# Performance work log

Measured on AMD Instinct MI355X. Metric: run time of the kernel, lower is better.

The kernel has to match this reference:

```python
import jax, jax.numpy as jnp
import numpy as np

D_MODEL = 1024
D_STATE = 16
D_CONV = 4
EXPAND = 2
D_INNER = EXPAND * D_MODEL
BATCH = 2
SEQ = 4096


def setup_inputs() -> dict:
    key = jax.random.key(0)
    ks = jax.random.split(key, 8)
    def w(k, shape, fan_in):
        return jax.random.normal(k, shape, jnp.float32) * (fan_in ** -0.5)
    x = jax.random.normal(ks[0], (BATCH, SEQ, D_MODEL), jnp.float32)
    in_proj_w = w(ks[1], (2 * D_INNER, D_MODEL), D_MODEL)
    conv_w = w(ks[2], (D_INNER, 1, D_CONV), D_CONV)          # depthwise conv kernel (OIH, groups=D_INNER)
    conv_b = jnp.zeros((D_INNER,), jnp.float32)
    x_proj_w = w(ks[3], (1 + 2 * D_STATE, D_INNER), D_INNER)
    dt_proj_w = w(ks[4], (D_INNER, 1), D_STATE)               # Linear(1 -> d_inner), see notes
    dt_proj_b = jnp.zeros((D_INNER,), jnp.float32)
    A_log = jnp.log(jnp.tile(jnp.arange(1, D_STATE + 1, dtype=jnp.float32)[None, :], (D_INNER, 1)))
    D = jnp.ones((D_INNER,), jnp.float32)
    out_proj_w = w(ks[5], (D_MODEL, D_INNER), D_INNER)
    return dict(x=x, in_proj_w=in_proj_w, conv_w=conv_w, conv_b=conv_b,
                x_proj_w=x_proj_w, dt_proj_w=dt_proj_w, dt_proj_b=dt_proj_b,
                A_log=A_log, D=D, out_proj_w=out_proj_w)


def _selective_scan(xs, delta, Bm, Cm, A, D):
    # xs, delta: [B, L, d_inner]; Bm, Cm: [B, L, d_state]; A: [d_inner, d_state]
    def step(h, inp):
        x_t, d_t, b_t, c_t = inp                      # [B,di],[B,di],[B,n],[B,n]
        dA = jnp.exp(d_t[..., None] * A)              # [B, di, n]
        h = dA * h + (d_t * x_t)[..., None] * b_t[:, None, :]
        y = jnp.einsum('bdn,bn->bd', h, c_t) + D * x_t
        return h, y
    h0 = jnp.zeros((xs.shape[0], xs.shape[2], A.shape[1]), xs.dtype)
    seq = (jnp.swapaxes(xs, 0, 1), jnp.swapaxes(delta, 0, 1),
           jnp.swapaxes(Bm, 0, 1), jnp.swapaxes(Cm, 0, 1))
    _, ys = jax.lax.scan(step, h0, seq)               # ys: [L, B, di]
    return jnp.swapaxes(ys, 0, 1)


def _mamba(x, in_proj_w, conv_w, conv_b, x_proj_w, dt_proj_w, dt_proj_b, A_log, D, out_proj_w):
    xz = x @ in_proj_w.T                               # [B, L, 2*di]
    xc, z = jnp.split(xz, 2, axis=-1)
    # causal depthwise conv (pad left d_conv-1, truncate to seq_len)
    u = jnp.swapaxes(xc, 1, 2)                         # [B, di, L]
    u = jax.lax.conv_general_dilated(
        u, conv_w, window_strides=(1,), padding=[(D_CONV - 1, 0)],
        feature_group_count=D_INNER, dimension_numbers=('NCH', 'OIH', 'NCH'))
    u = u + conv_b[None, :, None]
    xs = jax.nn.silu(jnp.swapaxes(u, 1, 2))            # [B, L, di]
    dbc = xs @ x_proj_w.T                              # [B, L, 1+2n]
    delta_raw = dbc[..., :1]
    Bm = dbc[..., 1:1 + D_STATE]
    Cm = dbc[..., 1 + D_STATE:]
    delta = jax.nn.softplus(delta_raw @ dt_proj_w.T + dt_proj_b)   # [B, L, di]
    A = -jnp.exp(A_log)
    y = _selective_scan(xs, delta, Bm, Cm, A, D)
    return (y * jax.nn.silu(z)) @ out_proj_w.T


def reference(x, in_proj_w, conv_w, conv_b, x_proj_w, dt_proj_w, dt_proj_b, A_log, D, out_proj_w):
    return _mamba(x, in_proj_w, conv_w, conv_b, x_proj_w, dt_proj_w, dt_proj_b, A_log, D, out_proj_w)
```

## Files before the change

### kernel.cpp

```cpp
#include <hip/hip_runtime.h>
#include <hip/hip_bf16.h>
#include <stdint.h>

typedef __bf16 bf16x8 __attribute__((ext_vector_type(8)));
typedef float  f32x4  __attribute__((ext_vector_type(4)));
typedef unsigned short u16x8 __attribute__((ext_vector_type(8)));

#define TC 64
#define NC 64
#define TH 32

__device__ __forceinline__ unsigned short f2bf(float f) {
  unsigned u = __builtin_bit_cast(unsigned, f);
  unsigned r = (u + 0x7fffu + ((u >> 16) & 1u)) >> 16;
  return (unsigned short)r;
}
__device__ __forceinline__ float bf2f(unsigned short s) {
  unsigned u = ((unsigned)s) << 16;
  return __builtin_bit_cast(float, u);
}

__device__ __forceinline__ void gload_lds16(const void* g, void* l) {
  __builtin_amdgcn_global_load_lds(
      (const __attribute__((address_space(1))) unsigned int*)(g),
      (__attribute__((address_space(3))) unsigned int*)(l),
      16, 0, 0);
}

__device__ __forceinline__ void rpowers(float r, float* rp) {
  float r2 = r * r, r4 = r2 * r2, r8 = r4 * r4;
  rp[0] = r;        rp[1] = r2;       rp[2] = r2 * r;   rp[3] = r4;
  rp[4] = r4 * r;   rp[5] = r4 * r2;  rp[6] = rp[5] * r; rp[7] = r8;
  rp[8] = r8 * r;   rp[9] = r8 * r2;  rp[10] = rp[9] * r; rp[11] = r8 * r4;
  rp[12] = rp[11] * r; rp[13] = rp[11] * r2; rp[14] = rp[13] * r; rp[15] = r8 * r8;
}

__global__ __launch_bounds__(256) void cast_bf16_k(const float4* __restrict__ in,
                                                   ushort4* __restrict__ out, int n4) {
  int i = blockIdx.x * 256 + threadIdx.x;
  int stride = gridDim.x * 256;
  for (; i < n4; i += stride) {
    float4 v = in[i];
    ushort4 o;
    o.x = f2bf(v.x); o.y = f2bf(v.y); o.z = f2bf(v.z); o.w = f2bf(v.w);
    out[i] = o;
  }
}

__global__ __launch_bounds__(256) void pad_xw_k(const float* __restrict__ xw,
                                                unsigned short* __restrict__ xwp) {
  int i = blockIdx.x * 256 + threadIdx.x;
  if (i >= 128 * 2048) return;
  int row = i >> 11, col = i & 2047;
  xwp[i] = (row < 33) ? f2bf(xw[row * 2048 + col]) : (unsigned short)0;
}

template <bool BF16OUT, bool SWZ>
__global__ __launch_bounds__(256) void gemm2p(
    const unsigned short* __restrict__ A, const unsigned short* __restrict__ B,
    void* __restrict__ Cv, int M, int N, int K)
{
  __shared__ __align__(16) unsigned short AsB[3 * 128 * 32];
  __shared__ __align__(16) unsigned short BsB[3 * 128 * 32];
  const int tid = threadIdx.x;

  const int grid_m = M >> 7, grid_n = N >> 7;
  const int nwg = grid_m * grid_n;
  int wid = blockIdx.x;
  if (SWZ) { int q = nwg >> 3; wid = (wid & 7) * q + (wid >> 3); }
  const int GM = 16;
  const int nig = GM * grid_n;
  const int gidg = wid / nig;
  const int rem = wid - gidg * nig;
  const int fm = gidg * GM;
  const int gsz = min(grid_m - fm, GM);
  const int pm = fm + rem % gsz;
  const int pn = rem / gsz;
  const int m0 = pm << 7, n0 = pn << 7;

  const int kseg = K / gridDim.z;
  const int kbeg = blockIdx.z * kseg;
  const int NT = kseg >> 5;

  const int w = tid >> 6, l = tid & 63;
  const int wr = w >> 1, wc = w & 1;
  const int lr = l & 15, kk = (l >> 4) * 8;

  f32x4 acc[4][4];
#pragma unroll
  for (int mi = 0; mi < 4; ++mi)
#pragma unroll
    for (int ni = 0; ni < 4; ++ni)
      acc[mi][ni] = (f32x4){0.f, 0.f, 0.f, 0.f};

#pragma unroll
  for (int tt = 0; tt < 2; ++tt) {
    unsigned short* as = AsB + tt * 4096;
    unsigned short* bs = BsB + tt * 4096;
    int k0 = kbeg + tt * 32;
#pragma unroll
    for (int i = 0; i < 2; ++i) {
      int q = tid + 256 * i;
      int row = q >> 2, sub = (q & 3) ^ ((q >> 3) & 3);
      gload_lds16(A + (size_t)(m0 + row) * K + k0 + sub * 8, as + q * 8);
      gload_lds16(B + (size_t)(n0 + row) * K + k0 + sub * 8, bs + q * 8);
    }
  }
  asm volatile("s_waitcnt vmcnt(4)\n\ts_barrier" ::: "memory");

  for (int t = 0; t < NT; ++t) {
    if (t + 2 < NT) {
      unsigned short* as = AsB + ((t + 2) % 3) * 4096;
      unsigned short* bs = BsB + ((t + 2) % 3) * 4096;
      int k0 = kbeg + (t + 2) * 32;
#pragma unroll
      for (int i = 0; i < 2; ++i) {
        int q = tid + 256 * i;
        int row = q >> 2, sub = (q & 3) ^ ((q >> 3) & 3);
        gload_lds16(A + (size_t)(m0 + row) * K + k0 + sub * 8, as + q * 8);
        gload_lds16(B + (size_t)(n0 + row) * K + k0 + sub * 8, bs + q * 8);
      }
    }
    const unsigned short* as = AsB + (t % 3) * 4096;
    const unsigned short* bs = BsB + (t % 3) * 4096;
    bf16x8 af[4], bfr[4];
#pragma unroll
    for (int mi = 0; mi < 4; ++mi) {
      int row = wr * 64 + mi * 16 + lr;
      int col = kk ^ (((row >> 1) & 3) << 3);
      af[mi] = *(const bf16x8*)&as[row * 32 + col];
    }
#pragma unroll
    for (int ni = 0; ni < 4; ++ni) {
      int row = wc * 64 + ni * 16 + lr;
      int col = kk ^ (((row >> 1) & 3) << 3);
      bfr[ni] = *(const bf16x8*)&bs[row * 32 + col];
    }
    __builtin_amdgcn_s_setprio(1);
#pragma unroll
    for (int mi = 0; mi < 4; ++mi)
#pragma unroll
      for (int ni = 0; ni < 4; ++ni)
        acc[mi][ni] = __builtin_amdgcn_mfma_f32_16x16x32_bf16(af[mi], bfr[ni], acc[mi][ni], 0, 0, 0);
    __builtin_amdgcn_s_setprio(0);
    if (t + 1 < NT) {
      if (t + 2 < NT) asm volatile("s_waitcnt vmcnt(4)\n\ts_barrier" ::: "memory");
      else            asm volatile("s_waitcnt vmcnt(0)\n\ts_barrier" ::: "memory");
    }
  }

#pragma unroll
  for (int mi = 0; mi < 4; ++mi)
#pragma unroll
    for (int ni = 0; ni < 4; ++ni) {
      int gr = m0 + wr * 64 + mi * 16 + (l >> 4) * 4;
      int gc = n0 + wc * 64 + ni * 16 + (l & 15);
#pragma unroll
      for (int j = 0; j < 4; ++j) {
        if (BF16OUT)
          ((unsigned short*)Cv)[(size_t)(gr + j) * N + gc] = f2bf(acc[mi][ni][j]);
        else
          ((float*)Cv + (size_t)blockIdx.z * M * N)[(size_t)(gr + j) * N + gc] = acc[mi][ni][j];
      }
    }
}

__global__ __launch_bounds__(256) void redux4_k(const float4* __restrict__ part,
                                                float4* __restrict__ out) {
  int i = blockIdx.x * 256 + threadIdx.x;
  const int STR = 262144;
  float4 a = part[i], b = part[i + STR], c = part[i + 2 * STR], d = part[i + 3 * STR];
  out[i] = make_float4(a.x + b.x + c.x + d.x, a.y + b.y + c.y + d.y,
                       a.z + b.z + c.z + d.z, a.w + b.w + c.w + d.w);
}

#define CONV_L 16
__global__ __launch_bounds__(256) void conv_silu_k(
    const unsigned short* __restrict__ xzb, const float* __restrict__ cw,
    const float* __restrict__ cb, unsigned short* __restrict__ xsb)
{
  const int b = blockIdx.y;
  const int l0 = blockIdx.x * CONV_L;
  const int d = threadIdx.x * 8;
  float w[4][8], bias[8];
#pragma unroll
  for (int i = 0; i < 8; ++i) {
    bias[i] = cb[d + i];
#pragma unroll
    for (int j = 0; j < 4; ++j) w[j][i] = cw[(d + i) * 4 + j];
  }
  const size_t rb = (size_t)b * 4096;
  float win[3][8];
#pragma unroll
  for (int j = 0; j < 3; ++j) {
    int l = l0 - 3 + j;
    if (l >= 0) {
      u16x8 v = *(const u16x8*)(xzb + (rb + l) * 4096 + d);
#pragma unroll
      for (int i = 0; i < 8; ++i) win[j][i] = bf2f(v[i]);
    } else {
#pragma unroll
      for (int i = 0; i < 8; ++i) win[j][i] = 0.f;
    }
  }
  for (int l = l0; l < l0 + CONV_L; ++l) {
    u16x8 v = *(const u16x8*)(xzb + (rb + l) * 4096 + d);
    float cur[8]; u16x8 ob;
#pragma unroll
    for (int i = 0; i < 8; ++i) {
      cur[i] = bf2f(v[i]);
      float u = bias[i] + w[0][i] * win[0][i] + w[1][i] * win[1][i]
                        + w[2][i] * win[2][i] + w[3][i] * cur[i];
      float s = u / (1.f + __expf(-u));
      ob[i] = f2bf(s);
    }
    *(u16x8*)(xsb + (rb + l) * 2048 + d) = ob;
#pragma unroll
    for (int i = 0; i < 8; ++i) { win[0][i] = win[1][i]; win[1][i] = win[2][i]; win[2][i] = cur[i]; }
  }
}

__global__ __launch_bounds__(256) void scan_p1(
    const unsigned short* __restrict__ xsb16, const float* __restrict__ dbc,
    const float* __restrict__ dtw, const float* __restrict__ dtb,
    const float* __restrict__ alog,
    float* __restrict__ Sg, float* __restrict__ cdg)
{
  const int chunk = blockIdx.x;
  const int d0 = blockIdx.y * 256;
  const int b = blockIdx.z;
  const int tid = threadIdx.x;
  const size_t rowbase = (size_t)b * 4096 + chunk * TC;

  __shared__ __align__(16) unsigned short xsS[TH][256];
  __shared__ __align__(16) float bS[TC][16];
  __shared__ float drS[TC];

  if (tid < TC) drS[tid] = dbc[(rowbase + tid) * 128];
  for (int i = tid; i < TC * 16; i += 256) {
    int t = i >> 4, q = i & 15;
    bS[t][q] = dbc[(rowbase + t) * 128 + 1 + q];
  }

  const int d = d0 + tid;
  const float wdt = dtw[d], bdt = dtb[d];
  float adn[16];
  bool ok = true;
#pragma unroll
  for (int k = 0; k < 4; ++k) {
    float4 a4 = *(const float4*)(alog + (size_t)d * 16 + k * 4);
    adn[4 * k + 0] = -__expf(a4.x); adn[4 * k + 1] = -__expf(a4.y);
    adn[4 * k + 2] = -__expf(a4.z); adn[4 * k + 3] = -__expf(a4.w);
  }
#pragma unroll
  for (int n = 0; n < 16; ++n)
    ok = ok && (fabsf(adn[n] + (float)(n + 1)) <= 1e-3f * (float)(n + 1));

  float h[16];
#pragma unroll
  for (int n = 0; n < 16; ++n) h[n] = 0.f;
  float cd = 0.f;

  for (int half = 0; half < 2; ++half) {
    if (half) __syncthreads();
    for (int i = tid; i < TH * 32; i += 256) {
      int tt = i >> 5, q = i & 31;
      *(u16x8*)&xsS[tt][q * 8] =
          *(const u16x8*)(xsb16 + (rowbase + half * TH + tt) * 2048 + d0 + q * 8);
    }
    __syncthreads();

    if (ok) {
      for (int tt = 0; tt < TH; ++tt) {
        int t = half * TH + tt;
        float pre = fmaf(drS[t], wdt, bdt);
        float e = __expf(pre);
        float dlt = (pre > 20.f) ? pre : __logf(1.f + e);
        float xv = bf2f(xsS[tt][tid]);
        float dx = dlt * xv;
        cd += dlt;
        float r = __expf(-dlt);
        float rp[16];
        rpowers(r, rp);
        f32x4 Bv[4];
#pragma unroll
        for (int k = 0; k < 4; ++k) Bv[k] = ((const f32x4*)&bS[t][0])[k];
#pragma unroll
        for (int n = 0; n < 16; ++n)
          h[n] = fmaf(rp[n], h[n], dx * Bv[n >> 2][n & 3]);
      }
    } else {
      for (int tt = 0; tt < TH; ++tt) {
        int t = half * TH + tt;
        float pre = fmaf(drS[t], wdt, bdt);
        float e = __expf(pre);
        float dlt = (pre > 20.f) ? pre : __logf(1.f + e);
        float xv = bf2f(xsS[tt][tid]);
        float dx = dlt * xv;
        cd += dlt;
        f32x4 Bv[4];
#pragma unroll
        for (int k = 0; k < 4; ++k) Bv[k] = ((const f32x4*)&bS[t][0])[k];
#pragma unroll
        for (int n = 0; n < 16; ++n) {
          float dA = __expf(adn[n] * dlt);
          h[n] = fmaf(dA, h[n], dx * Bv[n >> 2][n & 3]);
        }
      }
    }
  }
  cdg[(size_t)(b * NC + chunk) * 2048 + d] = cd;
  float* Sp = Sg + ((size_t)(b * NC + chunk) * 32768 + (size_t)d * 16);
#pragma unroll
  for (int k = 0; k < 4; ++k)
    ((float4*)Sp)[k] = make_float4(h[4 * k], h[4 * k + 1], h[4 * k + 2], h[4 * k + 3]);
}

__global__ __launch_bounds__(256) void scan_p2(
    const float* __restrict__ Sg, const float* __restrict__ cdg,
    const float* __restrict__ alog, float* __restrict__ Hg)
{
  int g = blockIdx.x * 256 + threadIdx.x;
  int b = g >> 15, dn = g & 32767;
  int d = dn >> 4;
  float adn = -__expf(alog[dn]);
  float h = 0.f;
  for (int c = 0; c < NC; ++c) {
    size_t o = (size_t)(b * NC + c) * 32768 + dn;
    float P = __expf(adn * cdg[(size_t)(b * NC + c) * 2048 + d]);
    Hg[o] = h;
    h = fmaf(P, h, Sg[o]);
  }
}

__global__ __launch_bounds__(256) void scan_p3(
    const unsigned short* __restrict__ xsb16, const float* __restrict__ dbc,
    const float* __restrict__ dtw, const float* __restrict__ dtb,
    const float* __restrict__ alog, const float* __restrict__ Dp,
    const unsigned short* __restrict__ xzb, const float* __restrict__ Hg,
    unsigned short* __restrict__ gb)
{
  const int chunk = blockIdx.x;
  const int d0 = blockIdx.y * 256;
  const int b = blockIdx.z;
  const int tid = threadIdx.x;
  const size_t rowbase = (size_t)b * 4096 + chunk * TC;

  __shared__ __align__(16) unsigned short xsS[TH][256];
  __shared__ __align__(16) float bcS[TC][32];

  for (int i = tid; i < TC * 32; i += 256) {
    int t = i >> 5, q = i & 31;
    bcS[t][q] = dbc[(rowbase + t) * 128 + 1 + q];
  }

  const int d = d0 + tid;
  const float wdt = dtw[d], bdt = dtb[d], Dd = Dp[d];
  const float* __restrict__ drp = dbc + rowbase * 128;
  float adn[16];
  bool ok = true;
#pragma unroll
  for (int k = 0; k < 4; ++k) {
    float4 a4 = *(const float4*)(alog + (size_t)d * 16 + k * 4);
    adn[4 * k + 0] = -__expf(a4.x); adn[4 * k + 1] = -__expf(a4.y);
    adn[4 * k + 2] = -__expf(a4.z); adn[4 * k + 3] = -__expf(a4.w);
  }
#pragma unroll
  for (int n = 0; n < 16; ++n)
    ok = ok && (fabsf(adn[n] + (float)(n + 1)) <= 1e-3f * (float)(n + 1));

  float h[16];
  {
    const float* Hp = Hg + ((size_t)(b * NC + chunk) * 32768 + (size_t)d * 16);
#pragma unroll
    for (int k = 0; k < 4; ++k) {
      float4 h4 = ((const float4*)Hp)[k];
      h[4 * k + 0] = h4.x; h[4 * k + 1] = h4.y; h[4 * k + 2] = h4.z; h[4 * k + 3] = h4.w;
    }
  }

  for (int half = 0; half < 2; ++half) {
    if (half) __syncthreads();
    for (int i = tid; i < TH * 32; i += 256) {
      int tt = i >> 5, q = i & 31;
      *(u16x8*)&xsS[tt][q * 8] =
          *(const u16x8*)(xsb16 + (rowbase + half * TH + tt) * 2048 + d0 + q * 8);
    }
    __syncthreads();

    if (ok) {
      for (int tt = 0; tt < TH; ++tt) {
        int t = half * TH + tt;
        float pre = fmaf(drp[(size_t)t * 128], wdt, bdt);
        float e = __expf(pre);
        float dlt = (pre > 20.f) ? pre : __logf(1.f + e);
        float xv = bf2f(xsS[tt][tid]);
        float dx = dlt * xv;
        float r = __expf(-dlt);
        float rp[16];
        rpowers(r, rp);
        f32x4 Bv[4], Cv[4];
#pragma unroll
        for (int k = 0; k < 4; ++k) {
          Bv[k] = ((const f32x4*)&bcS[t][0])[k];
          Cv[k] = ((const f32x4*)&bcS[t][16])[k];
        }
        float yp[4];
        yp[0] = Dd * xv; yp[1] = 0.f; yp[2] = 0.f; yp[3] = 0.f;
#pragma unroll
        for (int n = 0; n < 16; ++n) {
          h[n] = fmaf(rp[n], h[n], dx * Bv[n >> 2][n & 3]);
          yp[n & 3] = fmaf(h[n], Cv[n >> 2][n & 3], yp[n & 3]);
        }
        float y = (yp[0] + yp[1]) + (yp[2] + yp[3]);
        xsS[tt][tid] = f2bf(y);
      }
    } else {
      for (int tt = 0; tt < TH; ++tt) {
        int t = half * TH + tt;
        float pre = fmaf(drp[(size_t)t * 128], wdt, bdt);
        float e = __expf(pre);
        float dlt = (pre > 20.f) ? pre : __logf(1.f + e);
        float xv = bf2f(xsS[tt][tid]);
        float dx = dlt * xv;
        f32x4 Bv[4], Cv[4];
#pragma unroll
        for (int k = 0; k < 4; ++k) {
          Bv[k] = ((const f32x4*)&bcS[t][0])[k];
          Cv[k] = ((const f32x4*)&bcS[t][16])[k];
        }
        float yp[4];
        yp[0] = Dd * xv; yp[1] = 0.f; yp[2] = 0.f; yp[3] = 0.f;
#pragma unroll
        for (int n = 0; n < 16; ++n) {
          float dA = __expf(adn[n] * dlt);
          h[n] = fmaf(dA, h[n], dx * Bv[n >> 2][n & 3]);
          yp[n & 3] = fmaf(h[n], Cv[n >> 2][n & 3], yp[n & 3]);
        }
        float y = (yp[0] + yp[1]) + (yp[2] + yp[3]);
        xsS[tt][tid] = f2bf(y);
      }
    }
    __syncthreads();

    for (int i = tid; i < TH * 32; i += 256) {
      int tt = i >> 5, q = i & 31;
      size_t row = rowbase + half * TH + tt;
      u16x8 yv = *(const u16x8*)&xsS[tt][q * 8];
      u16x8 zv = *(const u16x8*)(xzb + row * 4096 + 2048 + d0 + q * 8);
      u16x8 ov;
#pragma unroll
      for (int j = 0; j < 8; ++j) {
        float z = bf2f(zv[j]);
        float s = z / (1.f + __expf(-z));
        ov[j] = f2bf(bf2f(yv[j]) * s);
      }
      *(u16x8*)(gb + row * 2048 + d0 + q * 8) = ov;
    }
  }
}

extern "C" void kernel_launch(void* const* d_in, const int* in_sizes, int n_in,
                              void* d_out, int out_size, void* d_ws, size_t ws_size,
                              hipStream_t stream) {
  const float* x    = (const float*)d_in[0];
  const float* ipw  = (const float*)d_in[1];
  const float* cw   = (const float*)d_in[2];
  const float* cb   = (const float*)d_in[3];
  const float* xpw  = (const float*)d_in[4];
  const float* dtw  = (const float*)d_in[5];
  const float* dtb  = (const float*)d_in[6];
  const float* alog = (const float*)d_in[7];
  const float* Dp   = (const float*)d_in[8];
  const float* opw  = (const float*)d_in[9];
  float* out = (float*)d_out;

  char* p = (char*)d_ws;
  unsigned short* xb   = (unsigned short*)p; p += (size_t)8388608 * 2;
  unsigned short* wb1  = (unsigned short*)p; p += (size_t)4194304 * 2;
  unsigned short* wb2  = (unsigned short*)p; p += (size_t)2097152 * 2;
  unsigned short* xwp  = (unsigned short*)p; p += (size_t)262144 * 2;
  unsigned short* xzb  = (unsigned short*)p; p += (size_t)33554432 * 2;
  unsigned short* xsb16= (unsigned short*)p; p += (size_t)16777216 * 2;
  float*          dbc  = (float*)p;          p += (size_t)1048576 * 4;
  unsigned short* gb   = (unsigned short*)p; p += (size_t)16777216 * 2;
  float*          Sg   = (float*)p;          p += (size_t)4194304 * 4;
  float*          cdg  = (float*)p;          p += (size_t)262144 * 4;
  float*          Hg   = (float*)xb;
  float*          dbcp = Sg;

  cast_bf16_k<<<1024, 256, 0, stream>>>((const float4*)x,   (ushort4*)xb,  8388608 / 4);
  cast_bf16_k<<<1024, 256, 0, stream>>>((const float4*)ipw, (ushort4*)wb1, 4194304 / 4);
  cast_bf16_k<<<512,  256, 0, stream>>>((const float4*)opw, (ushort4*)wb2, 2097152 / 4);
  pad_xw_k<<<1024, 256, 0, stream>>>(xpw, xwp);

  gemm2p<true, true><<<2048, 256, 0, stream>>>(xb, wb1, xzb, 8192, 4096, 1024);
  conv_silu_k<<<dim3(4096 / CONV_L, 2), 256, 0, stream>>>(xzb, cw, cb, xsb16);

  gemm2p<false, false><<<dim3(64, 1, 4), 256, 0, stream>>>(xsb16, xwp, dbcp, 8192, 128, 2048);
  redux4_k<<<1024, 256, 0, stream>>>((const float4*)dbcp, (float4*)dbc);

  scan_p1<<<dim3(NC, 8, 2), 256, 0, stream>>>(xsb16, dbc, dtw, dtb, alog, Sg, cdg);
  scan_p2<<<256, 256, 0, stream>>>(Sg, cdg, alog, Hg);
  scan_p3<<<dim3(NC, 8, 2), 256, 0, stream>>>(xsb16, dbc, dtw, dtb, alog, Dp, xzb, Hg, gb);

  gemm2p<false, true><<<512, 256, 0, stream>>>(gb, wb2, out, 8192, 1024, 2048);
}
```

Measured before the change: 307.0 us.

## Add 256x256-tile 8-wave GEMM with quadrant-pipelined staging for in_proj

Adds a new GEMM kernel using 512 threads and 256x256 output tiles with K-step 64, double-buffered LDS split into half-tiles. Loads of the next half-tiles are interleaved with MFMA on the current quadrants, with barriers and priority hints between them. It replaces the 128x128 GEMM for the in_proj matmul (8192x4096x1024) to raise data reuse per load and overlap memory with compute. In exchange it uses far more registers and LDS per block and adds many barriers, which could cut occupancy.

Result: faster. 295.2 us (-3.9%).

```diff
diff --git a/kernel.cpp b/kernel.cpp
--- a/kernel.cpp
+++ b/kernel.cpp
@@ -56,6 +56,145 @@
 }
 
 template <bool BF16OUT, bool SWZ>
+__global__ __launch_bounds__(512) void gemm8p(
+    const unsigned short* __restrict__ A, const unsigned short* __restrict__ B,
+    void* __restrict__ Cv, int M, int N, int K)
+{
+  __shared__ __align__(16) unsigned short As[2][2][8192];
+  __shared__ __align__(16) unsigned short Bs[2][2][8192];
+  const int tid = threadIdx.x;
+
+  const int grid_m = M >> 8, grid_n = N >> 8;
+  const int nwg = grid_m * grid_n;
+  int wid = blockIdx.x;
+  if (SWZ) { int q = nwg >> 3; wid = (wid & 7) * q + (wid >> 3); }
+  const int GM = 8;
+  const int nig = GM * grid_n;
+  const int gidg = wid / nig;
+  const int rem = wid - gidg * nig;
+  const int fm = gidg * GM;
+  const int gsz = (grid_m - fm < GM) ? (grid_m - fm) : GM;
+  const int pm = fm + rem % gsz;
+  const int pn = rem / gsz;
+  const int m0 = pm << 8, n0 = pn << 8;
+
+  const int NT = K >> 6;
+
+  const int wq = tid >> 6, l = tid & 63;
+  const int wr2 = wq >> 2, wc2 = wq & 3;
+  const int lr = l & 15, q16 = l >> 4;
+  const int sw = lr & 7;
+
+  const unsigned short* aH0 = A + (size_t)m0 * K;
+  const unsigned short* aH1 = A + (size_t)(m0 + 128) * K;
+  const unsigned short* bH0 = B + (size_t)n0 * K;
+  const unsigned short* bH1 = B + (size_t)(n0 + 128) * K;
+
+#define STAGE8(srcbase, dstp, kt)                                              \
+  { _Pragma("unroll") for (int i = 0; i < 2; ++i) {                            \
+      int q = tid + 512 * i; int rw = q >> 3; int ssl = (q & 7) ^ (rw & 7);    \
+      gload_lds16((srcbase) + (size_t)rw * K + (size_t)(kt) * 64 + ssl * 8,    \
+                  (dstp) + q * 8); } }
+
+#define LDA8(dd, MH)                                                           \
+  { _Pragma("unroll") for (int mi = 0; mi < 4; ++mi) {                         \
+      int ar = (wr2 * 64 + mi * 16 + lr) * 64;                                 \
+      _Pragma("unroll") for (int ks = 0; ks < 2; ++ks)                         \
+        af[mi][ks] = *(const bf16x8*)&As[dd][MH][ar + (((ks * 4 + q16) ^ sw) << 3)]; } }
+
+#define LDB8(dd, NH)                                                           \
+  { _Pragma("unroll") for (int ni = 0; ni < 2; ++ni) {                         \
+      int br = (wc2 * 32 + ni * 16 + lr) * 64;                                 \
+      _Pragma("unroll") for (int ks = 0; ks < 2; ++ks)                         \
+        bf[NH][ni][ks] = *(const bf16x8*)&Bs[dd][NH][br + (((ks * 4 + q16) ^ sw) << 3)]; } }
+
+#define MMA8(MH, NH)                                                           \
+  { __builtin_amdgcn_s_setprio(1);                                             \
+    _Pragma("unroll") for (int mi = 0; mi < 4; ++mi)                           \
+    _Pragma("unroll") for (int ni = 0; ni < 2; ++ni)                           \
+    _Pragma("unroll") for (int ks = 0; ks < 2; ++ks)                           \
+      acc[MH][NH][mi][ni] = __builtin_amdgcn_mfma_f32_16x16x32_bf16(           \
+          af[mi][ks], bf[NH][ni][ks], acc[MH][NH][mi][ni], 0, 0, 0);           \
+    __builtin_amdgcn_s_setprio(0); }
+
+  f32x4 acc[2][2][4][2];
+#pragma unroll
+  for (int a = 0; a < 2; ++a)
+#pragma unroll
+    for (int b = 0; b < 2; ++b)
+#pragma unroll
+      for (int c = 0; c < 4; ++c)
+#pragma unroll
+        for (int d = 0; d < 2; ++d)
+          acc[a][b][c][d] = (f32x4){0.f, 0.f, 0.f, 0.f};
+
+  bf16x8 af[4][2];
+  bf16x8 bf[2][2][2];
+
+  STAGE8(aH0, As[0][0], 0);
+  STAGE8(bH1, Bs[0][1], 0);
+  STAGE8(aH1, As[0][1], 0);
+  STAGE8(bH0, Bs[0][0], 0);
+  if (NT > 1) {
+    STAGE8(aH0, As[1][0], 1);
+    STAGE8(bH1, Bs[1][1], 1);
+    asm volatile("s_waitcnt vmcnt(4)" ::: "memory");
+  } else {
+    asm volatile("s_waitcnt vmcnt(0)" ::: "memory");
+  }
+  __builtin_amdgcn_s_barrier();
+
+  for (int t = 0; t < NT; ++t) {
+    const int d = t & 1;
+    LDA8(d, 0); LDB8(d, 0);
+    if (t + 1 < NT) STAGE8(aH1, As[(t + 1) & 1][1], t + 1);
+    __builtin_amdgcn_s_barrier();
+    MMA8(0, 0);
+    __builtin_amdgcn_s_barrier();
+    LDB8(d, 1);
+    if (t + 1 < NT) STAGE8(bH0, Bs[(t + 1) & 1][0], t + 1);
+    __builtin_amdgcn_s_barrier();
+    MMA8(0, 1);
+    __builtin_amdgcn_s_barrier();
+    LDA8(d, 1);
+    if (t + 2 < NT) STAGE8(aH0, As[d][0], t + 2);
+    __builtin_amdgcn_s_barrier();
+    MMA8(1, 1);
+    __builtin_amdgcn_s_barrier();
+    if (t + 2 < NT) STAGE8(bH1, Bs[d][1], t + 2);
+    __builtin_amdgcn_s_barrier();
+    MMA8(1, 0);
+    __builtin_amdgcn_s_barrier();
+    if (t + 2 < NT) asm volatile("s_waitcnt vmcnt(4)" ::: "memory");
+    else            asm volatile("s_waitcnt vmcnt(0)" ::: "memory");
+    __builtin_amdgcn_s_barrier();
+  }
+
+#pragma unroll
+  for (int mh = 0; mh < 2; ++mh)
+#pragma unroll
+    for (int nh = 0; nh < 2; ++nh)
+#pragma unroll
+      for (int mi = 0; mi < 4; ++mi)
+#pragma unroll
+        for (int ni = 0; ni < 2; ++ni) {
+          int gr = m0 + mh * 128 + wr2 * 64 + mi * 16 + q16 * 4;
+          int gc = n0 + nh * 128 + wc2 * 32 + ni * 16 + lr;
+#pragma unroll
+          for (int j = 0; j < 4; ++j) {
+            if (BF16OUT)
+              ((unsigned short*)Cv)[(size_t)(gr + j) * N + gc] = f2bf(acc[mh][nh][mi][ni][j]);
+            else
+              ((float*)Cv)[(size_t)(gr + j) * N + gc] = acc[mh][nh][mi][ni][j];
+          }
+        }
+#undef STAGE8
+#undef LDA8
+#undef LDB8
+#undef MMA8
+}
+
+template <bool BF16OUT, bool SWZ>
 __global__ __launch_bounds__(256) void gemm2p(
     const unsigned short* __restrict__ A, const unsigned short* __restrict__ B,
     void* __restrict__ Cv, int M, int N, int K)
@@ -73,7 +212,7 @@
   const int gidg = wid / nig;
   const int rem = wid - gidg * nig;
   const int fm = gidg * GM;
-  const int gsz = min(grid_m - fm, GM);
+  const int gsz = (grid_m - fm < GM) ? (grid_m - fm) : GM;
   const int pm = fm + rem % gsz;
   const int pn = rem / gsz;
   const int m0 = pm << 7, n0 = pn << 7;
@@ -494,7 +633,7 @@
   cast_bf16_k<<<512,  256, 0, stream>>>((const float4*)opw, (ushort4*)wb2, 2097152 / 4);
   pad_xw_k<<<1024, 256, 0, stream>>>(xpw, xwp);
 
-  gemm2p<true, true><<<2048, 256, 0, stream>>>(xb, wb1, xzb, 8192, 4096, 1024);
+  gemm8p<true, true><<<512, 512, 0, stream>>>(xb, wb1, xzb, 8192, 4096, 1024);
   conv_silu_k<<<dim3(4096 / CONV_L, 2), 256, 0, stream>>>(xzb, cw, cb, xsb16);
 
   gemm2p<false, false><<<dim3(64, 1, 4), 256, 0, stream>>>(xsb16, xwp, dbcp, 8192, 128, 2048);
@@ -504,5 +643,5 @@
   scan_p2<<<256, 256, 0, stream>>>(Sg, cdg, alog, Hg);
   scan_p3<<<dim3(NC, 8, 2), 256, 0, stream>>>(xsb16, dbc, dtw, dtb, alog, Dp, xzb, Hg, gb);
 
-  gemm2p<false, true><<<512, 256, 0, stream>>>(gb, wb2, out, 8192, 1024, 2048);
-}
+  gemm2p<false, true><<<dim3(512, 1, 1), 256, 0, stream>>>(gb, wb2, out, 8192, 1024, 2048);
+}
```
